# Optimization experiments

Measured on AMD Instinct MI355X. Metric: run time of the kernel, lower is better.

The kernel has to match this reference:

```python
import jax, jax.numpy as jnp
import numpy as np

N = 500000      # number of active voxels (same coords in/out: stride 1)
C_IN = 32
C_OUT = 32
K = 27          # 3x3x3 kernel volume
M = 250000      # neighbors per kernel offset (fixed for jit-ability)


def setup_inputs() -> dict:
    key = jax.random.key(0)
    k1, k2, k3, k4 = jax.random.split(key, 4)
    feats = jax.random.normal(k1, (N, C_IN), dtype=jnp.float32)
    std = 1.0 / np.sqrt(C_IN * K)
    weight = jax.random.uniform(k2, (K, C_IN, C_OUT), dtype=jnp.float32,
                                minval=-std, maxval=std)
    in_idx = jax.random.randint(k3, (K, M), 0, N, dtype=jnp.int32)
    out_idx = jax.random.randint(k4, (K, M), 0, N, dtype=jnp.int32)
    return {"feats": feats, "weight": weight, "in_idx": in_idx, "out_idx": out_idx}


def reference(feats, weight, in_idx, out_idx):
    # gather: [K, M, C_in]
    gathered = feats[in_idx]
    # per-offset matmul: [K, M, C_out]
    edge_out = jnp.einsum('kmc,kcd->kmd', gathered, weight)
    # scatter-add into output rows: [N, C_out]
    out = jnp.zeros((feats.shape[0], weight.shape[-1]), dtype=feats.dtype)
    out = out.at[out_idx.reshape(-1)].add(edge_out.reshape(-1, weight.shape[-1]))
    return out
```

## Files before the change

### kernel.cpp

```cpp
#include <hip/hip_runtime.h>

#define C_IN   32
#define C_OUT  32
#define K_VOL  27
#define M_EDGE 250000
#define N_ROWS 500000
#define E_TOT  (K_VOL * M_EDGE)

#define NT        (N_ROWS / 16)
#define NREG      977
#define BPB       16
#define CHUNK     (M_EDGE / BPB)
#define OSTRIDE   (NREG + 1)
#define NSEG      (K_VOL * BPB)
#define NLISTS    512
#define CAPL      16
#define LSTRIDE   17

#define NCVT      2048
#define NI_F      (N_ROWS * C_IN / 8)
#define NI_W      (K_VOL * C_IN * C_OUT)

typedef __attribute__((ext_vector_type(8))) short s16x8;
typedef __attribute__((ext_vector_type(4))) float f32x4;

static __device__ __forceinline__ unsigned short f2bf(float x) {
    union { float f; unsigned int u; } c; c.f = x;
    const unsigned int r = (c.u + 0x7FFFu + ((c.u >> 16) & 1u)) >> 16;
    return (unsigned short)r;
}
static __device__ __forceinline__ unsigned int cvtpk(float lo, float hi) {
    unsigned int r;
    asm("v_cvt_pk_bf16_f32 %0, %1, %2" : "=v"(r) : "v"(lo), "v"(hi));
    return r;
}
static __device__ __forceinline__ void unpack_add(float2* af, const s16x8& f) {
    union { s16x8 v; unsigned int w[4]; } u; u.v = f;
#pragma unroll
    for (int d = 0; d < 4; ++d) {
        af[d].x += __uint_as_float(u.w[d] << 16);
        af[d].y += __uint_as_float(u.w[d] & 0xffff0000u);
    }
}

__global__ __launch_bounds__(256) void prep_kernel(
    const float* __restrict__ feats, const float* __restrict__ weight,
    const int* __restrict__ in_idx, const int* __restrict__ out_idx,
    unsigned short* __restrict__ feats16, unsigned short* __restrict__ wT16,
    int* __restrict__ lstartG, unsigned int* __restrict__ edge_buf)
{
    __shared__ int lh[NREG];
    __shared__ int lstart[NREG + 1];
    __shared__ int lcur[NREG];
    __shared__ int partial[256];
    __shared__ unsigned int pay[CHUNK];
    const int bx = blockIdx.x, tid = threadIdx.x;

    if (bx >= NSEG) {
        const int id0 = (bx - NSEG) * 256 + tid;
        const int stride = NCVT * 256;
        for (int i = id0; i < NI_F; i += stride) {
            const float4 v0 = reinterpret_cast<const float4*>(feats)[i * 2];
            const float4 v1 = reinterpret_cast<const float4*>(feats)[i * 2 + 1];
            s16x8 r;
            r[0] = (short)f2bf(v0.x); r[1] = (short)f2bf(v0.y);
            r[2] = (short)f2bf(v0.z); r[3] = (short)f2bf(v0.w);
            r[4] = (short)f2bf(v1.x); r[5] = (short)f2bf(v1.y);
            r[6] = (short)f2bf(v1.z); r[7] = (short)f2bf(v1.w);
            *reinterpret_cast<s16x8*>(feats16 + (size_t)i * 8) = r;
        }
        if (id0 < NI_W) {
            const int k = id0 >> 10, rem = id0 & 1023;
            const int co = rem >> 5, ci = rem & 31;
            wT16[id0] = f2bf(weight[k * 1024 + ci * 32 + co]);
        }
        return;
    }

    const int blk = bx & 15, k = bx >> 4;
    const int seg = k * BPB + blk;

    for (int r = tid; r < NREG; r += 256) lh[r] = 0;
    __syncthreads();

    const int eb0 = k * M_EDGE + blk * CHUNK;
    const int* ob = out_idx + eb0;
    const int* ib = in_idx + eb0;

    for (int t = tid; t < CHUNK; t += 256)
        atomicAdd(&lh[ob[t] >> 9], 1);
    __syncthreads();

    int psum = 0;
    const int r0 = tid * 4;
#pragma unroll
    for (int j = 0; j < 4; ++j) { const int r = r0 + j; if (r < NREG) psum += lh[r]; }
    partial[tid] = psum;
    __syncthreads();
    for (int off = 1; off < 256; off <<= 1) {
        const int t = (tid >= off) ? partial[tid - off] : 0;
        __syncthreads();
        partial[tid] += t;
        __syncthreads();
    }
    int run = partial[tid] - psum;
#pragma unroll
    for (int j = 0; j < 4; ++j) {
        const int r = r0 + j;
        if (r < NREG) { lstart[r] = run; lcur[r] = run; run += lh[r]; }
    }
    if (tid == 0) lstart[NREG] = CHUNK;
    __syncthreads();

    for (int r = tid; r <= NREG; r += 256)
        lstartG[seg * OSTRIDE + r] = lstart[r];

    for (int t = tid; t < CHUNK; t += 256) {
        const int row = ob[t];
        const int irow = ib[t];
        const int idx = atomicAdd(&lcur[row >> 9], 1);
        pay[idx] = (unsigned int)irow | ((unsigned int)(row & 15) << 19) |
                   ((unsigned int)((row >> 4) & 31) << 23);
    }
    __syncthreads();

    unsigned int* dst = edge_buf + (size_t)seg * CHUNK;
    for (int q = tid; q < CHUNK; q += 256)
        dst[q] = pay[q];
}

__global__ __launch_bounds__(512, 4) void conv_mfma12(
    const unsigned short* __restrict__ feats16,
    const unsigned short* __restrict__ wT16,
    const int* __restrict__ lstartG,
    const unsigned int* __restrict__ edge_buf,
    float* __restrict__ out)
{
    __shared__ int lcnt[2 * NLISTS];
    __shared__ unsigned int lists[NLISTS * LSTRIDE];
    __shared__ int lsAll[NSEG * 2];
    const int g = blockIdx.x;
    const int tid = threadIdx.x;
    const int lane = tid & 63, wv = tid >> 6;
    const int slot = lane & 15, chunk = lane >> 4;

    for (int i = tid; i < NSEG * 2; i += 512)
        lsAll[i] = lstartG[(i >> 1) * OSTRIDE + g + (i & 1)];
    lcnt[tid] = 0;
    lcnt[tid + NLISTS] = 0;

    f32x4 a0[4], a1[4];
#pragma unroll
    for (int j = 0; j < 4; ++j) {
        a0[j] = (f32x4){0.f, 0.f, 0.f, 0.f};
        a1[j] = (f32x4){0.f, 0.f, 0.f, 0.f};
    }
    __syncthreads();

#pragma unroll 1
    for (int k = 0; k < K_VOL; ++k) {
        const int cb = (k & 1) * NLISTS;

        const int bb = tid >> 5, u = tid & 31;
        const int sB = lsAll[(k * BPB + bb) * 2], eB = lsAll[(k * BPB + bb) * 2 + 1];
        const unsigned int* ebp = edge_buf + (size_t)(k * BPB + bb) * CHUNK;
        for (int t = sB + u; t < eB; t += 32) {
            const unsigned int p = ebp[t];
            const int li = (int)((p >> 19) & 0x1FFu);
            const int idx = atomicAdd(&lcnt[cb + li], 1);
            if (idx < CAPL) lists[li * LSTRIDE + idx] = p & 0x7FFFFu;
        }
        __syncthreads();

        lcnt[(cb ^ NLISTS) + tid] = 0;

        const unsigned short* wk = wT16 + k * (C_IN * C_OUT);
        const s16x8 b0 = *reinterpret_cast<const s16x8*>(wk + slot * 32 + chunk * 8);
        const s16x8 b1 = *reinterpret_cast<const s16x8*>(wk + (slot + 16) * 32 + chunk * 8);

        int myc[4]; unsigned int e0[4], e1[4], e2[4];
#pragma unroll
        for (int j = 0; j < 4; ++j) {
            const int li = (wv * 4 + j) * 16 + slot;
            const int c = lcnt[cb + li];
            myc[j] = c > CAPL ? CAPL : c;
            e0[j] = lists[li * LSTRIDE];
            e1[j] = lists[li * LSTRIDE + 1];
            e2[j] = lists[li * LSTRIDE + 2];
        }
        s16x8 g0[4], g1[4], g2[4];
#pragma unroll
        for (int j = 0; j < 4; ++j) {
            g0[j] = (s16x8){0, 0, 0, 0, 0, 0, 0, 0};
            g1[j] = (s16x8){0, 0, 0, 0, 0, 0, 0, 0};
            g2[j] = (s16x8){0, 0, 0, 0, 0, 0, 0, 0};
        }
#pragma unroll
        for (int j = 0; j < 4; ++j)
            if (0 < myc[j])
                g0[j] = *reinterpret_cast<const s16x8*>(
                    feats16 + (size_t)e0[j] * C_IN + chunk * 8);
#pragma unroll
        for (int j = 0; j < 4; ++j)
            if (1 < myc[j])
                g1[j] = *reinterpret_cast<const s16x8*>(
                    feats16 + (size_t)e1[j] * C_IN + chunk * 8);
#pragma unroll
        for (int j = 0; j < 4; ++j)
            if (2 < myc[j])
                g2[j] = *reinterpret_cast<const s16x8*>(
                    feats16 + (size_t)e2[j] * C_IN + chunk * 8);

#pragma unroll
        for (int j = 0; j < 4; ++j) {
            union { unsigned int w[4]; s16x8 v; } A;
            if (!__any(myc[j] > 1)) {
                A.v = g0[j];
            } else {
                float2 af[4];
#pragma unroll
                for (int d = 0; d < 4; ++d) af[d] = make_float2(0.f, 0.f);
                unpack_add(af, g0[j]);
                unpack_add(af, g1[j]);
                unpack_add(af, g2[j]);
                const int li = (wv * 4 + j) * 16 + slot;
#pragma unroll 1
                for (int i = 3; __any(i < myc[j]); ++i) {
                    s16x8 f = {0, 0, 0, 0, 0, 0, 0, 0};
                    if (i < myc[j])
                        f = *reinterpret_cast<const s16x8*>(
                            feats16 + (size_t)lists[li * LSTRIDE + i] * C_IN + chunk * 8);
                    unpack_add(af, f);
                }
#pragma unroll
                for (int d = 0; d < 4; ++d) A.w[d] = cvtpk(af[d].x, af[d].y);
            }
            a0[j] = __builtin_amdgcn_mfma_f32_16x16x32_bf16(A.v, b0, a0[j], 0, 0, 0);
            a1[j] = __builtin_amdgcn_mfma_f32_16x16x32_bf16(A.v, b1, a1[j], 0, 0, 0);
        }
        __syncthreads();
    }

#pragma unroll
    for (int j = 0; j < 4; ++j) {
        const int rtg = g * 32 + wv * 4 + j;
        if (rtg < NT) {
            const int r0 = rtg * 16 + chunk * 4;
#pragma unroll
            for (int jj = 0; jj < 4; ++jj) {
                out[(size_t)(r0 + jj) * C_OUT + slot]      = a0[j][jj];
                out[(size_t)(r0 + jj) * C_OUT + 16 + slot] = a1[j][jj];
            }
        }
    }
}

__global__ __launch_bounds__(256) void spconv_edges(
    const float* __restrict__ feats, const float* __restrict__ weight,
    const int* __restrict__ in_idx, const int* __restrict__ out_idx,
    float* __restrict__ out)
{
    const int k = blockIdx.y;
    const int tid = threadIdx.x;
    const int g = tid >> 3, l = tid & 7, c0 = l * 4;
    const float* wk = weight + k * (C_IN * C_OUT);
    float4 wr[32];
#pragma unroll
    for (int ci = 0; ci < 32; ++ci)
        wr[ci] = *reinterpret_cast<const float4*>(wk + ci * C_OUT + c0);
    const int* ik = in_idx + k * M_EDGE;
    const int* ok = out_idx + k * M_EDGE;
    int m = blockIdx.x * 1024 + g;
#pragma unroll 1
    for (int it = 0; it < 32; ++it, m += 32) {
        if (m >= M_EDGE) break;
        const int irow = ik[m], orow = ok[m];
        const float4* frow =
            reinterpret_cast<const float4*>(feats + (size_t)irow * C_IN);
        float4 a = make_float4(0.f, 0.f, 0.f, 0.f);
#pragma unroll
        for (int j = 0; j < 8; ++j) {
            const float4 f4 = frow[j];
            const float fv[4] = {f4.x, f4.y, f4.z, f4.w};
#pragma unroll
            for (int t = 0; t < 4; ++t) {
                const float4 w4 = wr[j * 4 + t];
                a.x = fmaf(fv[t], w4.x, a.x);
                a.y = fmaf(fv[t], w4.y, a.y);
                a.z = fmaf(fv[t], w4.z, a.z);
                a.w = fmaf(fv[t], w4.w, a.w);
            }
        }
        float* op = out + (size_t)orow * C_OUT + c0;
        unsafeAtomicAdd(op + 0, a.x);
        unsafeAtomicAdd(op + 1, a.y);
        unsafeAtomicAdd(op + 2, a.z);
        unsafeAtomicAdd(op + 3, a.w);
    }
}

extern "C" void kernel_launch(void* const* d_in, const int* in_sizes, int n_in,
                              void* d_out, int out_size, void* d_ws, size_t ws_size,
                              hipStream_t stream) {
    const float* feats   = (const float*)d_in[0];
    const float* weight  = (const float*)d_in[1];
    const int*   in_idx  = (const int*)d_in[2];
    const int*   out_idx = (const int*)d_in[3];
    float*       out     = (float*)d_out;

    const size_t feats16_elems = (size_t)N_ROWS * C_IN;
    const size_t wT16_elems    = (size_t)K_VOL * C_IN * C_OUT;
    const size_t lstart_elems  = (size_t)NSEG * OSTRIDE;
    const size_t need_bytes = feats16_elems * 2 + wT16_elems * 2 +
        lstart_elems * sizeof(int) + (size_t)E_TOT * 4 + 256;

    if (ws_size >= need_bytes) {
        unsigned short* feats16 = (unsigned short*)d_ws;
        unsigned short* wT16    = feats16 + feats16_elems;
        int* lstartG = (int*)(wT16 + wT16_elems);
        unsigned int* edge_buf = (unsigned int*)(lstartG + lstart_elems);

        prep_kernel<<<NSEG + NCVT, 256, 0, stream>>>(
            feats, weight, in_idx, out_idx, feats16, wT16, lstartG, edge_buf);
        conv_mfma12<<<NREG, 512, 0, stream>>>(feats16, wT16, lstartG, edge_buf, out);
    } else {
        hipMemsetAsync(out, 0, (size_t)out_size * sizeof(float), stream);
        dim3 grid((M_EDGE + 1023) / 1024, K_VOL);
        spconv_edges<<<grid, dim3(256), 0, stream>>>(feats, weight, in_idx, out_idx, out);
    }
}
```

Before: 242.2 us.

## Software-pipeline edge list building one kernel offset ahead of MFMA compute

The per-offset loop now builds the bucketed neighbor lists for offset k+1 before running the gather and MFMA for offset k. This uses double-buffered lists and triple-buffered counters in LDS, so each iteration needs one barrier instead of two. The aim is to overlap edge-buffer loads and LDS atomics with the feature gathers and reduce barrier stalls. In exchange LDS use rises by about 35KB per block, which may lower occupancy below the four-blocks launch bound.

```diff
diff --git a/kernel.cpp b/kernel.cpp
--- a/kernel.cpp
+++ b/kernel.cpp
@@ -129,15 +129,15 @@
         dst[q] = pay[q];
 }
 
-__global__ __launch_bounds__(512, 4) void conv_mfma12(
+__global__ __launch_bounds__(512, 4) void conv_mfma13(
     const unsigned short* __restrict__ feats16,
     const unsigned short* __restrict__ wT16,
     const int* __restrict__ lstartG,
     const unsigned int* __restrict__ edge_buf,
     float* __restrict__ out)
 {
-    __shared__ int lcnt[2 * NLISTS];
-    __shared__ unsigned int lists[NLISTS * LSTRIDE];
+    __shared__ int lcnt[3 * NLISTS];
+    __shared__ unsigned int lists[2 * NLISTS * LSTRIDE];
     __shared__ int lsAll[NSEG * 2];
     const int g = blockIdx.x;
     const int tid = threadIdx.x;
@@ -148,6 +148,7 @@
         lsAll[i] = lstartG[(i >> 1) * OSTRIDE + g + (i & 1)];
     lcnt[tid] = 0;
     lcnt[tid + NLISTS] = 0;
+    lcnt[tid + 2 * NLISTS] = 0;
 
     f32x4 a0[4], a1[4];
 #pragma unroll
@@ -157,22 +158,39 @@
     }
     __syncthreads();
 
-#pragma unroll 1
-    for (int k = 0; k < K_VOL; ++k) {
-        const int cb = (k & 1) * NLISTS;
-
+    {
         const int bb = tid >> 5, u = tid & 31;
-        const int sB = lsAll[(k * BPB + bb) * 2], eB = lsAll[(k * BPB + bb) * 2 + 1];
-        const unsigned int* ebp = edge_buf + (size_t)(k * BPB + bb) * CHUNK;
+        const int sB = lsAll[bb * 2], eB = lsAll[bb * 2 + 1];
+        const unsigned int* ebp = edge_buf + (size_t)bb * CHUNK;
         for (int t = sB + u; t < eB; t += 32) {
             const unsigned int p = ebp[t];
             const int li = (int)((p >> 19) & 0x1FFu);
-            const int idx = atomicAdd(&lcnt[cb + li], 1);
+            const int idx = atomicAdd(&lcnt[li], 1);
             if (idx < CAPL) lists[li * LSTRIDE + idx] = p & 0x7FFFFu;
         }
-        __syncthreads();
-
-        lcnt[(cb ^ NLISTS) + tid] = 0;
+    }
+    __syncthreads();
+
+#pragma unroll 1
+    for (int k = 0; k < K_VOL; ++k) {
+        if (k + 1 < K_VOL) {
+            const int kn = k + 1;
+            const int cbn = (kn % 3) * NLISTS;
+            unsigned int* lstn = lists + (kn & 1) * (NLISTS * LSTRIDE);
+            const int bb = tid >> 5, u = tid & 31;
+            const int sB = lsAll[(kn * BPB + bb) * 2], eB = lsAll[(kn * BPB + bb) * 2 + 1];
+            const unsigned int* ebp = edge_buf + (size_t)(kn * BPB + bb) * CHUNK;
+            for (int t = sB + u; t < eB; t += 32) {
+                const unsigned int p = ebp[t];
+                const int li = (int)((p >> 19) & 0x1FFu);
+                const int idx = atomicAdd(&lcnt[cbn + li], 1);
+                if (idx < CAPL) lstn[li * LSTRIDE + idx] = p & 0x7FFFFu;
+            }
+        }
+        lcnt[((k + 2) % 3) * NLISTS + tid] = 0;
+
+        const int cb = (k % 3) * NLISTS;
+        const unsigned int* lst = lists + (k & 1) * (NLISTS * LSTRIDE);
 
         const unsigned short* wk = wT16 + k * (C_IN * C_OUT);
         const s16x8 b0 = *reinterpret_cast<const s16x8*>(wk + slot * 32 + chunk * 8);
@@ -184,9 +202,9 @@
             const int li = (wv * 4 + j) * 16 + slot;
             const int c = lcnt[cb + li];
             myc[j] = c > CAPL ? CAPL : c;
-            e0[j] = lists[li * LSTRIDE];
-            e1[j] = lists[li * LSTRIDE + 1];
-            e2[j] = lists[li * LSTRIDE + 2];
+            e0[j] = lst[li * LSTRIDE];
+            e1[j] = lst[li * LSTRIDE + 1];
+            e2[j] = lst[li * LSTRIDE + 2];
         }
         s16x8 g0[4], g1[4], g2[4];
 #pragma unroll
@@ -229,7 +247,7 @@
                     s16x8 f = {0, 0, 0, 0, 0, 0, 0, 0};
                     if (i < myc[j])
                         f = *reinterpret_cast<const s16x8*>(
-                            feats16 + (size_t)lists[li * LSTRIDE + i] * C_IN + chunk * 8);
+                            feats16 + (size_t)lst[li * LSTRIDE + i] * C_IN + chunk * 8);
                     unpack_add(af, f);
                 }
 #pragma unroll
@@ -322,7 +340,7 @@
 
         prep_kernel<<<NSEG + NCVT, 256, 0, stream>>>(
             feats, weight, in_idx, out_idx, feats16, wT16, lstartG, edge_buf);
-        conv_mfma12<<<NREG, 512, 0, stream>>>(feats16, wT16, lstartG, edge_buf, out);
+        conv_mfma13<<<NREG, 512, 0, stream>>>(feats16, wT16, lstartG, edge_buf, out);
     } else {
         hipMemsetAsync(out, 0, (size_t)out_size * sizeof(float), stream);
         dim3 grid((M_EDGE + 1023) / 1024, K_VOL);
```

After: 251.2 us. 1.04x slower.
